# Kernel optimization log

Measured on AMD Instinct MI355X. Metric: run time of the kernel, lower is better.

The kernel has to match this reference:

```python
import jax, jax.numpy as jnp
import numpy as np

B, S, H, NH = 4, 2048, 768, 12
HD = H // NH

def _ln(x, g, b, eps=1e-5):
    m = jnp.mean(x, -1, keepdims=True)
    v = jnp.mean((x - m) ** 2, -1, keepdims=True)
    return (x - m) * jax.lax.rsqrt(v + eps) * g + b

def setup_inputs() -> dict:
    key = jax.random.key(0)
    ks = jax.random.split(key, 16)
    s = 0.02
    return {
        "x": jax.random.normal(ks[0], (B, S, H), jnp.float32),
        "prev_state": jax.random.normal(ks[1], (B, S, H), jnp.float32),
        "mask": jax.random.randint(ks[2], (B,), 0, 2).astype(bool),
        # depthwise conv1d (groups=H, k=3): torch weight [H, 1, 3] == OIH
        "conv_dw_w": jax.random.normal(ks[3], (H, 1, 3), jnp.float32) * s,
        "conv_dw_b": jnp.zeros((H,), jnp.float32),
        # pointwise conv1d (k=1) stored as [out, in]
        "conv_pw_w": jax.random.normal(ks[4], (H, H), jnp.float32) * s,
        "conv_pw_b": jnp.zeros((H,), jnp.float32),
        "cn_g": jnp.ones((H,), jnp.float32), "cn_b": jnp.zeros((H,), jnp.float32),
        "Wq": jax.random.normal(ks[5], (H, H), jnp.float32) * s, "bq": jnp.zeros((H,), jnp.float32),
        "Wk": jax.random.normal(ks[6], (H, H), jnp.float32) * s, "bk": jnp.zeros((H,), jnp.float32),
        "Wv": jax.random.normal(ks[7], (H, H), jnp.float32) * s, "bv": jnp.zeros((H,), jnp.float32),
        "Wo": jax.random.normal(ks[8], (H, H), jnp.float32) * s, "bo": jnp.zeros((H,), jnp.float32),
        "pn_g": jnp.ones((H,), jnp.float32), "pn_b": jnp.zeros((H,), jnp.float32),
        "Wpost": jax.random.normal(ks[9], (H, H), jnp.float32) * s, "bpost": jnp.zeros((H,), jnp.float32),
        "Wg": jax.random.normal(ks[10], (1, 2 * H), jnp.float32) * s, "bg": jnp.zeros((1,), jnp.float32),
    }

def reference(x, prev_state, mask, conv_dw_w, conv_dw_b, conv_pw_w, conv_pw_b,
              cn_g, cn_b, Wq, bq, Wk, bk, Wv, bv, Wo, bo,
              pn_g, pn_b, Wpost, bpost, Wg, bg):
    # ---- bridge: depthwise conv (k=3) -> pointwise conv (k=1) -> GELU -> LN ----
    mem_t = prev_state.transpose(0, 2, 1)  # [B, H, S]
    dw = jax.lax.conv_general_dilated(
        mem_t, conv_dw_w, window_strides=(1,), padding=[(1, 1)],
        feature_group_count=H, dimension_numbers=("NCH", "OIH", "NCH")) + conv_dw_b[None, :, None]
    pw = jnp.einsum("bhs,oh->bos", dw, conv_pw_w) + conv_pw_b[None, :, None]
    bridged = jax.nn.gelu(pw, approximate=False).transpose(0, 2, 1)  # [B, S, H]
    bridged = _ln(bridged, cn_g, cn_b)
    # ---- cross attention: q from x, k/v from bridged memory (nope, non-causal) ----
    q = (jnp.einsum("bsh,oh->bso", x, Wq) + bq).reshape(B, S, NH, HD)
    k = (jnp.einsum("bsh,oh->bso", bridged, Wk) + bk).reshape(B, S, NH, HD)
    v = (jnp.einsum("bsh,oh->bso", bridged, Wv) + bv).reshape(B, S, NH, HD)
    scores = jnp.einsum("bqnd,bknd->bnqk", q, k) / np.float32(np.sqrt(HD))
    attn = jax.nn.softmax(scores, axis=-1)
    ao = jnp.einsum("bnqk,bknd->bqnd", attn, v).reshape(B, S, H)
    ao = jnp.einsum("bsh,oh->bso", ao, Wo) + bo
    # ---- post-attn norm, linear, gate, scatter-add back under mask ----
    inj = _ln(ao, pn_g, pn_b)
    inj = jnp.einsum("bsh,oh->bso", inj, Wpost) + bpost
    gate = jax.nn.sigmoid(jnp.einsum("bsh,oh->bso", jnp.concatenate([x, bridged], -1), Wg) + bg)
    gated = gate * jnp.tanh(inj)
    mf = mask.astype(x.dtype)[:, None, None]  # batch-row select == masked scatter-add
    out = x + mf * gated
    # masked MSE aux loss (only over selected rows, as in the original)
    denom = jnp.maximum(mask.sum(), 1).astype(x.dtype) * np.float32(S * H)
    aux = jnp.sum(mf * (bridged - x) ** 2) / denom
    return out, aux
```

## Files before the change

kernel.cpp:

```cpp
#include <hip/hip_runtime.h>
#include <math.h>

#define B_ 4
#define S_ 2048
#define H_ 768
#define NH_ 12
#define HD_ 64
#define BSH (B_ * S_ * H_)
#define NROWS (B_ * S_)
#define WSZ (H_ * H_)

typedef __attribute__((ext_vector_type(8))) short bf16x8;
typedef __attribute__((ext_vector_type(4))) short s16x4;
typedef __attribute__((ext_vector_type(4))) float f32x4;
typedef __attribute__((ext_vector_type(2))) unsigned u32x2;

__device__ __forceinline__ short f2bf(float f) {
  union { float f; unsigned u; } x; x.f = f;
  unsigned r = x.u + 0x7FFF + ((x.u >> 16) & 1);
  return (short)(r >> 16);
}
__device__ __forceinline__ float bf2f(short s) {
  union { unsigned u; float f; } x;
  x.u = ((unsigned)(unsigned short)s) << 16;
  return x.f;
}
__device__ __forceinline__ unsigned bfpack(float lo, float hi) {
  union { float f; unsigned u; } a, b; a.f = lo; b.f = hi;
  return __builtin_amdgcn_perm(b.u, a.u, 0x07060302);
}

typedef __attribute__((address_space(1))) const unsigned int g_u32;
typedef __attribute__((address_space(3))) unsigned int l_u32;
__device__ __forceinline__ void gload16(const void* g, void* l) {
  __builtin_amdgcn_global_load_lds((g_u32*)g, (l_u32*)l, 16, 0, 0);
}

__global__ __launch_bounds__(256) void cvt_x_k(const float* __restrict__ src,
                                               short* __restrict__ dst) {
  int i = (blockIdx.x * 256 + threadIdx.x) * 4;
  float4 v = *(const float4*)(src + i);
  s16x4 o = {f2bf(v.x), f2bf(v.y), f2bf(v.z), f2bf(v.w)};
  *(s16x4*)(dst + i) = o;
}

__global__ __launch_bounds__(256) void cvt6_k(const float* w0, const float* w1,
                                              const float* w2, const float* w3,
                                              const float* w4, const float* w5,
                                              short* __restrict__ dst) {
  int i = (blockIdx.x * 256 + threadIdx.x) * 4;
  int m = i / WSZ;
  int off = i - m * WSZ;
  const float* s = m == 0 ? w0 : m == 1 ? w1 : m == 2 ? w2 : m == 3 ? w3 : m == 4 ? w4 : w5;
  float4 v = *(const float4*)(s + off);
  s16x4 o = {f2bf(v.x), f2bf(v.y), f2bf(v.z), f2bf(v.w)};
  *(s16x4*)(dst + i) = o;
}

__global__ __launch_bounds__(256) void dwconv_k(const float* __restrict__ prev,
                                                const float* __restrict__ w3,
                                                const float* __restrict__ bias,
                                                short* __restrict__ out) {
  int row = blockIdx.x;
  int s = row & (S_ - 1);
  size_t base = (size_t)row * H_;
  for (int h = threadIdx.x; h < H_; h += 256) {
    float acc = bias[h] + prev[base + h] * w3[h * 3 + 1];
    if (s > 0)      acc += prev[base - H_ + h] * w3[h * 3 + 0];
    if (s < S_ - 1) acc += prev[base + H_ + h] * w3[h * 3 + 2];
    out[base + h] = f2bf(acc);
  }
}

__global__ __launch_bounds__(256) void gemm_bf(const short* __restrict__ A,
                                               const short* __restrict__ W,
                                               const float* __restrict__ bias,
                                               short* __restrict__ C,
                                               int act, int tout) {
  __shared__ short As[4096];
  __shared__ short Ws[4096];
  int tid = threadIdx.x, lane = tid & 63, w = tid >> 6;
  int wr = w >> 1, wc = w & 1, lm = lane & 15, lq = lane >> 4;
  int m0 = blockIdx.y * 128, n0 = blockIdx.x * 128;
  int srow = w * 32 + (lane >> 2);
  int skc = (lane & 3) * 8;
  const short* gA = A + (size_t)(m0 + srow) * H_ + skc;
  const short* gW = W + (size_t)(n0 + srow) * H_ + skc;
  short* lA = As + w * 1024;
  short* lW = Ws + w * 1024;

  f32x4 acc[4][4];
#pragma unroll
  for (int i = 0; i < 4; ++i)
#pragma unroll
    for (int j = 0; j < 4; ++j) acc[i][j] = (f32x4){0.f, 0.f, 0.f, 0.f};

  for (int kt = 0; kt < H_; kt += 32) {
    __syncthreads();
    gload16(gA + kt, lA);
    gload16(gA + kt + 16 * H_, lA + 512);
    gload16(gW + kt, lW);
    gload16(gW + kt + 16 * H_, lW + 512);
    __syncthreads();
    bf16x8 af[4], wf[4];
#pragma unroll
    for (int i = 0; i < 4; ++i) af[i] = *(const bf16x8*)&As[(wr * 64 + i * 16 + lm) * 32 + lq * 8];
#pragma unroll
    for (int j = 0; j < 4; ++j) wf[j] = *(const bf16x8*)&Ws[(wc * 64 + j * 16 + lm) * 32 + lq * 8];
#pragma unroll
    for (int i = 0; i < 4; ++i)
#pragma unroll
      for (int j = 0; j < 4; ++j)
        acc[i][j] = __builtin_amdgcn_mfma_f32_16x16x32_bf16(af[i], wf[j], acc[i][j], 0, 0, 0);
  }

  if (!tout) {
#pragma unroll
    for (int j = 0; j < 4; ++j) {
      int col = n0 + wc * 64 + j * 16 + lm;
      float bn = bias[col];
#pragma unroll
      for (int i = 0; i < 4; ++i) {
        int mrow = m0 + wr * 64 + i * 16 + lq * 4;
#pragma unroll
        for (int r = 0; r < 4; ++r) {
          float cv = acc[i][j][r] + bn;
          if (act) cv = 0.5f * cv * (1.0f + erff(cv * 0.70710678118f));
          C[(size_t)(mrow + r) * H_ + col] = f2bf(cv);
        }
      }
    }
  } else {
    int b = m0 >> 11;
    int sb = (m0 & (S_ - 1)) + wr * 64;
#pragma unroll
    for (int j = 0; j < 4; ++j) {
      int col = n0 + wc * 64 + j * 16 + lm;
      float bn = bias[col];
      short* cp = C + ((size_t)(b * H_ + col)) * S_;
#pragma unroll
      for (int i = 0; i < 4; ++i) {
        int s = sb + i * 16 + lq * 4;
        s16x4 pk = {f2bf(acc[i][j][0] + bn), f2bf(acc[i][j][1] + bn),
                    f2bf(acc[i][j][2] + bn), f2bf(acc[i][j][3] + bn)};
        *(s16x4*)(cp + s) = pk;
      }
    }
  }
}

__global__ __launch_bounds__(256) void ln_bf(const short* __restrict__ X,
                                             short* __restrict__ Y,
                                             const float* __restrict__ g,
                                             const float* __restrict__ bb) {
  int row = blockIdx.x;
  size_t base = (size_t)row * H_;
  int h0 = threadIdx.x, h1 = h0 + 256, h2 = h0 + 512;
  float x0 = bf2f(X[base + h0]), x1 = bf2f(X[base + h1]), x2 = bf2f(X[base + h2]);
  float s = x0 + x1 + x2;
  float s2 = x0 * x0 + x1 * x1 + x2 * x2;
  for (int off = 32; off > 0; off >>= 1) {
    s += __shfl_down(s, off);
    s2 += __shfl_down(s2, off);
  }
  __shared__ float sa[4], sq[4], st[2];
  int wid = threadIdx.x >> 6, lane = threadIdx.x & 63;
  if (lane == 0) { sa[wid] = s; sq[wid] = s2; }
  __syncthreads();
  if (threadIdx.x == 0) {
    float ts = sa[0] + sa[1] + sa[2] + sa[3];
    float ts2 = sq[0] + sq[1] + sq[2] + sq[3];
    float mean = ts * (1.0f / H_);
    float var = ts2 * (1.0f / H_) - mean * mean;
    st[0] = mean;
    st[1] = rsqrtf(var + 1e-5f);
  }
  __syncthreads();
  float mean = st[0], rstd = st[1];
  Y[base + h0] = f2bf((x0 - mean) * rstd * g[h0] + bb[h0]);
  Y[base + h1] = f2bf((x1 - mean) * rstd * g[h1] + bb[h1]);
  Y[base + h2] = f2bf((x2 - mean) * rstd * g[h2] + bb[h2]);
}

__global__ __launch_bounds__(512) void attn3_k(const short* __restrict__ qb,
                                               const short* __restrict__ kb,
                                               const short* __restrict__ vtb,
                                               short* __restrict__ aob) {
  __shared__ short Ks[64 * 72];
  __shared__ short Vt[64 * 72];
  __shared__ short Ps[8 * 16 * 72];
  int tid = threadIdx.x, lane = tid & 63, w = tid >> 6;
  int lm = lane & 15, lq = lane >> 4;
  int b = blockIdx.z, n = blockIdx.y, q0 = blockIdx.x * 128;
  int hoff = n * HD_;

  const short* qrow = qb + ((size_t)(b * S_ + q0 + w * 16 + lm)) * H_ + hoff;
  bf16x8 qf0 = *(const bf16x8*)(qrow + lq * 8);
  bf16x8 qf1 = *(const bf16x8*)(qrow + 32 + lq * 8);

  float l_ = 0.f;
  f32x4 o[4];
#pragma unroll
  for (int i = 0; i < 4; ++i) o[i] = (f32x4){0.f, 0.f, 0.f, 0.f};

  int r0 = tid >> 3, c0 = (tid & 7) * 8;
  const short* kg = kb + ((size_t)(b * S_)) * H_ + hoff;
  const short* vg = vtb + ((size_t)(b * H_ + hoff)) * S_;
  const float C1 = 0.1803368802f;

  bf16x8 kv = *(const bf16x8*)(kg + (size_t)r0 * H_ + c0);
  bf16x8 vv = *(const bf16x8*)(vg + (size_t)r0 * S_ + c0);

  for (int kt = 0; kt < S_; kt += 64) {
    __syncthreads();
    *(bf16x8*)&Ks[r0 * 72 + c0] = kv;
    *(bf16x8*)&Vt[r0 * 72 + c0] = vv;
    __syncthreads();
    if (kt + 64 < S_) {
      kv = *(const bf16x8*)(kg + (size_t)(kt + 64 + r0) * H_ + c0);
      vv = *(const bf16x8*)(vg + (size_t)r0 * S_ + kt + 64 + c0);
    }

    f32x4 st[4];
#pragma unroll
    for (int ni = 0; ni < 4; ++ni) {
      bf16x8 ka0 = *(const bf16x8*)&Ks[(ni * 16 + lm) * 72 + lq * 8];
      bf16x8 ka1 = *(const bf16x8*)&Ks[(ni * 16 + lm) * 72 + 32 + lq * 8];
      f32x4 z = (f32x4){0.f, 0.f, 0.f, 0.f};
      z = __builtin_amdgcn_mfma_f32_16x16x32_bf16(ka0, qf0, z, 0, 0, 0);
      st[ni] = __builtin_amdgcn_mfma_f32_16x16x32_bf16(ka1, qf1, z, 0, 0, 0);
    }

    float rs = 0.f;
#pragma unroll
    for (int ni = 0; ni < 4; ++ni) {
      float p0 = exp2f(st[ni][0] * C1);
      float p1 = exp2f(st[ni][1] * C1);
      float p2 = exp2f(st[ni][2] * C1);
      float p3 = exp2f(st[ni][3] * C1);
      rs += (p0 + p1) + (p2 + p3);
      u32x2 pk = {bfpack(p0, p1), bfpack(p2, p3)};
      *(u32x2*)&Ps[(w * 16 + lm) * 72 + ni * 16 + lq * 4] = pk;
    }
    rs += __shfl_xor(rs, 16);
    rs += __shfl_xor(rs, 32);
    l_ += rs;

    bf16x8 pf0 = *(const bf16x8*)&Ps[(w * 16 + lm) * 72 + lq * 8];
    bf16x8 pf1 = *(const bf16x8*)&Ps[(w * 16 + lm) * 72 + 32 + lq * 8];
#pragma unroll
    for (int nd = 0; nd < 4; ++nd) {
      bf16x8 va0 = *(const bf16x8*)&Vt[(nd * 16 + lm) * 72 + lq * 8];
      bf16x8 va1 = *(const bf16x8*)&Vt[(nd * 16 + lm) * 72 + 32 + lq * 8];
      o[nd] = __builtin_amdgcn_mfma_f32_16x16x32_bf16(va0, pf0, o[nd], 0, 0, 0);
      o[nd] = __builtin_amdgcn_mfma_f32_16x16x32_bf16(va1, pf1, o[nd], 0, 0, 0);
    }
  }

  float inv = 1.0f / l_;
  short* orow = aob + ((size_t)(b * S_ + q0 + w * 16 + lm)) * H_ + hoff;
#pragma unroll
  for (int nd = 0; nd < 4; ++nd) {
    s16x4 pk = {f2bf(o[nd][0] * inv), f2bf(o[nd][1] * inv),
                f2bf(o[nd][2] * inv), f2bf(o[nd][3] * inv)};
    *(s16x4*)(orow + nd * 16 + lq * 4) = pk;
  }
}

__global__ __launch_bounds__(256) void gate_out_k(const float* __restrict__ x,
                                                  const short* __restrict__ br,
                                                  const short* __restrict__ inj,
                                                  const int* __restrict__ mask,
                                                  const float* __restrict__ Wg,
                                                  const float* __restrict__ bg,
                                                  float* __restrict__ out,
                                                  float* __restrict__ paux) {
  int row = blockIdx.x;
  int b = row >> 11;
  size_t base = (size_t)row * H_;
  float dot = 0.f, aux = 0.f;
  for (int h = threadIdx.x; h < H_; h += 256) {
    float xv = x[base + h], bv = bf2f(br[base + h]);
    dot += xv * Wg[h] + bv * Wg[H_ + h];
    float d = bv - xv;
    aux += d * d;
  }
  for (int off = 32; off > 0; off >>= 1) {
    dot += __shfl_down(dot, off);
    aux += __shfl_down(aux, off);
  }
  __shared__ float sd[4], sx[4], gsh[2];
  int wid = threadIdx.x >> 6, lane = threadIdx.x & 63;
  if (lane == 0) { sd[wid] = dot; sx[wid] = aux; }
  __syncthreads();
  if (threadIdx.x == 0) {
    float td = sd[0] + sd[1] + sd[2] + sd[3];
    float ta = sx[0] + sx[1] + sx[2] + sx[3];
    gsh[0] = 1.0f / (1.0f + expf(-(td + bg[0])));
    gsh[1] = ta;
  }
  __syncthreads();
  float mf = (mask[b] != 0) ? 1.0f : 0.0f;
  float gm = gsh[0] * mf;
  for (int h = threadIdx.x; h < H_; h += 256) {
    float v = bf2f(inj[base + h]);
    float e = __expf(2.0f * v);
    float th = (e - 1.0f) / (e + 1.0f);
    out[base + h] = x[base + h] + gm * th;
  }
  if (threadIdx.x == 0) paux[row] = mf * gsh[1];
}

__global__ __launch_bounds__(256) void aux_reduce_k(const float* __restrict__ paux,
                                                    const int* __restrict__ mask,
                                                    float* __restrict__ outp) {
  float s = 0.f;
  for (int i = threadIdx.x; i < NROWS; i += 256) s += paux[i];
  for (int off = 32; off > 0; off >>= 1) s += __shfl_down(s, off);
  __shared__ float sw[4];
  int wid = threadIdx.x >> 6, lane = threadIdx.x & 63;
  if (lane == 0) sw[wid] = s;
  __syncthreads();
  if (threadIdx.x == 0) {
    float t = sw[0] + sw[1] + sw[2] + sw[3];
    int nm = (mask[0] != 0) + (mask[1] != 0) + (mask[2] != 0) + (mask[3] != 0);
    if (nm < 1) nm = 1;
    outp[0] = t / ((float)nm * (float)(S_ * H_));
  }
}

extern "C" void kernel_launch(void* const* d_in, const int* in_sizes, int n_in,
                              void* d_out, int out_size, void* d_ws, size_t ws_size,
                              hipStream_t stream) {
  const float* x     = (const float*)d_in[0];
  const float* prev  = (const float*)d_in[1];
  const int*   mask  = (const int*)d_in[2];
  const float* dw_w  = (const float*)d_in[3];
  const float* dw_b  = (const float*)d_in[4];
  const float* pw_w  = (const float*)d_in[5];
  const float* pw_b  = (const float*)d_in[6];
  const float* cn_g  = (const float*)d_in[7];
  const float* cn_b  = (const float*)d_in[8];
  const float* Wq    = (const float*)d_in[9];
  const float* bq    = (const float*)d_in[10];
  const float* Wk    = (const float*)d_in[11];
  const float* bk    = (const float*)d_in[12];
  const float* Wv    = (const float*)d_in[13];
  const float* bv    = (const float*)d_in[14];
  const float* Wo    = (const float*)d_in[15];
  const float* bo    = (const float*)d_in[16];
  const float* pn_g  = (const float*)d_in[17];
  const float* pn_b  = (const float*)d_in[18];
  const float* Wpost = (const float*)d_in[19];
  const float* bpost = (const float*)d_in[20];
  const float* Wg    = (const float*)d_in[21];
  const float* bg    = (const float*)d_in[22];
  float* out = (float*)d_out;

  short* B0 = (short*)d_ws;
  short* B1 = B0 + BSH;
  short* B2 = B1 + BSH;
  short* B3 = B2 + BSH;
  short* B4 = B3 + BSH;
  short* B5 = B4 + BSH;
  short* WW = B5 + BSH;
  float* paux = (float*)(WW + 6 * WSZ);

  dim3 ggrid(H_ / 128, NROWS / 128);

  cvt6_k<<<6 * WSZ / 1024, 256, 0, stream>>>(pw_w, Wq, Wk, Wv, Wo, Wpost, WW);
  cvt_x_k<<<BSH / 1024, 256, 0, stream>>>(x, B0);
  dwconv_k<<<NROWS, 256, 0, stream>>>(prev, dw_w, dw_b, B1);
  gemm_bf<<<ggrid, 256, 0, stream>>>(B1, WW, pw_b, B2, 1, 0);
  ln_bf<<<NROWS, 256, 0, stream>>>(B2, B3, cn_g, cn_b);
  gemm_bf<<<ggrid, 256, 0, stream>>>(B0, WW + WSZ, bq, B1, 0, 0);
  gemm_bf<<<ggrid, 256, 0, stream>>>(B3, WW + 2 * WSZ, bk, B4, 0, 0);
  gemm_bf<<<ggrid, 256, 0, stream>>>(B3, WW + 3 * WSZ, bv, B5, 0, 1);
  attn3_k<<<dim3(S_ / 128, NH_, B_), 512, 0, stream>>>(B1, B4, B5, B2);
  gemm_bf<<<ggrid, 256, 0, stream>>>(B2, WW + 4 * WSZ, bo, B4, 0, 0);
  ln_bf<<<NROWS, 256, 0, stream>>>(B4, B4, pn_g, pn_b);
  gemm_bf<<<ggrid, 256, 0, stream>>>(B4, WW + 5 * WSZ, bpost, B5, 0, 0);
  gate_out_k<<<NROWS, 256, 0, stream>>>(x, B3, B5, mask, Wg, bg, out, paux);
  aux_reduce_k<<<1, 256, 0, stream>>>(paux, mask, out + BSH);
}
```

Measured before the change: 438.6 us.

## Batch QKV GEMMs in one launch, deepen K tile, vectorize elementwise kernels

The GEMM kernel now stages a 64-wide K slice per iteration instead of 32, which halves the number of barrier pairs. The Q, K and V projections are merged into a single launch using blockIdx.z to pick among three job descriptors. The depthwise conv and gate/output kernels now use 192 threads, each handling four contiguous elements with float4 and short4 loads instead of strided scalar loops. Together these aim to cut launch count, synchronisation overhead and memory instruction count, at the cost of twice the LDS per GEMM block, which may reduce occupancy.

```diff
diff --git a/kernel.cpp b/kernel.cpp
--- a/kernel.cpp
+++ b/kernel.cpp
@@ -57,76 +57,98 @@
   *(s16x4*)(dst + i) = o;
 }
 
-__global__ __launch_bounds__(256) void dwconv_k(const float* __restrict__ prev,
+__global__ __launch_bounds__(192) void dwconv_k(const float* __restrict__ prev,
                                                 const float* __restrict__ w3,
                                                 const float* __restrict__ bias,
                                                 short* __restrict__ out) {
   int row = blockIdx.x;
   int s = row & (S_ - 1);
-  size_t base = (size_t)row * H_;
-  for (int h = threadIdx.x; h < H_; h += 256) {
-    float acc = bias[h] + prev[base + h] * w3[h * 3 + 1];
-    if (s > 0)      acc += prev[base - H_ + h] * w3[h * 3 + 0];
-    if (s < S_ - 1) acc += prev[base + H_ + h] * w3[h * 3 + 2];
-    out[base + h] = f2bf(acc);
-  }
-}
-
-__global__ __launch_bounds__(256) void gemm_bf(const short* __restrict__ A,
-                                               const short* __restrict__ W,
-                                               const float* __restrict__ bias,
-                                               short* __restrict__ C,
-                                               int act, int tout) {
-  __shared__ short As[4096];
-  __shared__ short Ws[4096];
+  int h = threadIdx.x * 4;
+  size_t base = (size_t)row * H_ + h;
+  float4 c = *(const float4*)(prev + base);
+  float4 wa = *(const float4*)(w3 + h * 3);
+  float4 wb = *(const float4*)(w3 + h * 3 + 4);
+  float4 wc = *(const float4*)(w3 + h * 3 + 8);
+  float4 bi = *(const float4*)(bias + h);
+  float4 acc;
+  acc.x = bi.x + c.x * wa.y;
+  acc.y = bi.y + c.y * wb.x;
+  acc.z = bi.z + c.z * wb.w;
+  acc.w = bi.w + c.w * wc.z;
+  if (s > 0) {
+    float4 l = *(const float4*)(prev + base - H_);
+    acc.x += l.x * wa.x; acc.y += l.y * wa.w; acc.z += l.z * wb.z; acc.w += l.w * wc.y;
+  }
+  if (s < S_ - 1) {
+    float4 r = *(const float4*)(prev + base + H_);
+    acc.x += r.x * wa.z; acc.y += r.y * wb.y; acc.z += r.z * wc.x; acc.w += r.w * wc.w;
+  }
+  s16x4 o = {f2bf(acc.x), f2bf(acc.y), f2bf(acc.z), f2bf(acc.w)};
+  *(s16x4*)(out + base) = o;
+}
+
+struct GemmJob {
+  const short* A; const short* W; const float* bias; short* C; int act; int tout;
+};
+
+__global__ __launch_bounds__(256) void gemm_bf2(GemmJob j0, GemmJob j1, GemmJob j2) {
+  GemmJob j = blockIdx.z == 0 ? j0 : (blockIdx.z == 1 ? j1 : j2);
+  __shared__ short As[128 * 64];
+  __shared__ short Ws[128 * 64];
   int tid = threadIdx.x, lane = tid & 63, w = tid >> 6;
   int wr = w >> 1, wc = w & 1, lm = lane & 15, lq = lane >> 4;
   int m0 = blockIdx.y * 128, n0 = blockIdx.x * 128;
-  int srow = w * 32 + (lane >> 2);
-  int skc = (lane & 3) * 8;
-  const short* gA = A + (size_t)(m0 + srow) * H_ + skc;
-  const short* gW = W + (size_t)(n0 + srow) * H_ + skc;
-  short* lA = As + w * 1024;
-  short* lW = Ws + w * 1024;
+  int srow = lane >> 3;
+  int skc = (lane & 7) * 8;
+  const short* gA = j.A + (size_t)(m0 + w * 32 + srow) * H_ + skc;
+  const short* gW = j.W + (size_t)(n0 + w * 32 + srow) * H_ + skc;
+  short* lA = As + w * 2048;
+  short* lW = Ws + w * 2048;
 
   f32x4 acc[4][4];
 #pragma unroll
   for (int i = 0; i < 4; ++i)
 #pragma unroll
-    for (int j = 0; j < 4; ++j) acc[i][j] = (f32x4){0.f, 0.f, 0.f, 0.f};
-
-  for (int kt = 0; kt < H_; kt += 32) {
+    for (int jj = 0; jj < 4; ++jj) acc[i][jj] = (f32x4){0.f, 0.f, 0.f, 0.f};
+
+  for (int kt = 0; kt < H_; kt += 64) {
     __syncthreads();
-    gload16(gA + kt, lA);
-    gload16(gA + kt + 16 * H_, lA + 512);
-    gload16(gW + kt, lW);
-    gload16(gW + kt + 16 * H_, lW + 512);
+#pragma unroll
+    for (int c = 0; c < 4; ++c) {
+      gload16(gA + kt + (size_t)(c * 8) * H_, lA + c * 512);
+      gload16(gW + kt + (size_t)(c * 8) * H_, lW + c * 512);
+    }
     __syncthreads();
-    bf16x8 af[4], wf[4];
-#pragma unroll
-    for (int i = 0; i < 4; ++i) af[i] = *(const bf16x8*)&As[(wr * 64 + i * 16 + lm) * 32 + lq * 8];
-#pragma unroll
-    for (int j = 0; j < 4; ++j) wf[j] = *(const bf16x8*)&Ws[(wc * 64 + j * 16 + lm) * 32 + lq * 8];
-#pragma unroll
-    for (int i = 0; i < 4; ++i)
-#pragma unroll
-      for (int j = 0; j < 4; ++j)
-        acc[i][j] = __builtin_amdgcn_mfma_f32_16x16x32_bf16(af[i], wf[j], acc[i][j], 0, 0, 0);
-  }
-
-  if (!tout) {
-#pragma unroll
-    for (int j = 0; j < 4; ++j) {
-      int col = n0 + wc * 64 + j * 16 + lm;
-      float bn = bias[col];
+#pragma unroll
+    for (int kk = 0; kk < 2; ++kk) {
+      bf16x8 af[4], wf[4];
+#pragma unroll
+      for (int i = 0; i < 4; ++i)
+        af[i] = *(const bf16x8*)&As[(wr * 64 + i * 16 + lm) * 64 + kk * 32 + lq * 8];
+#pragma unroll
+      for (int jj = 0; jj < 4; ++jj)
+        wf[jj] = *(const bf16x8*)&Ws[(wc * 64 + jj * 16 + lm) * 64 + kk * 32 + lq * 8];
+#pragma unroll
+      for (int i = 0; i < 4; ++i)
+#pragma unroll
+        for (int jj = 0; jj < 4; ++jj)
+          acc[i][jj] = __builtin_amdgcn_mfma_f32_16x16x32_bf16(af[i], wf[jj], acc[i][jj], 0, 0, 0);
+    }
+  }
+
+  if (!j.tout) {
+#pragma unroll
+    for (int jj = 0; jj < 4; ++jj) {
+      int col = n0 + wc * 64 + jj * 16 + lm;
+      float bn = j.bias[col];
 #pragma unroll
       for (int i = 0; i < 4; ++i) {
         int mrow = m0 + wr * 64 + i * 16 + lq * 4;
 #pragma unroll
         for (int r = 0; r < 4; ++r) {
-          float cv = acc[i][j][r] + bn;
-          if (act) cv = 0.5f * cv * (1.0f + erff(cv * 0.70710678118f));
-          C[(size_t)(mrow + r) * H_ + col] = f2bf(cv);
+          float cv = acc[i][jj][r] + bn;
+          if (j.act) cv = 0.5f * cv * (1.0f + erff(cv * 0.70710678118f));
+          j.C[(size_t)(mrow + r) * H_ + col] = f2bf(cv);
         }
       }
     }
@@ -134,15 +156,15 @@
     int b = m0 >> 11;
     int sb = (m0 & (S_ - 1)) + wr * 64;
 #pragma unroll
-    for (int j = 0; j < 4; ++j) {
-      int col = n0 + wc * 64 + j * 16 + lm;
-      float bn = bias[col];
-      short* cp = C + ((size_t)(b * H_ + col)) * S_;
+    for (int jj = 0; jj < 4; ++jj) {
+      int col = n0 + wc * 64 + jj * 16 + lm;
+      float bn = j.bias[col];
+      short* cp = j.C + ((size_t)(b * H_ + col)) * S_;
 #pragma unroll
       for (int i = 0; i < 4; ++i) {
         int s = sb + i * 16 + lq * 4;
-        s16x4 pk = {f2bf(acc[i][j][0] + bn), f2bf(acc[i][j][1] + bn),
-                    f2bf(acc[i][j][2] + bn), f2bf(acc[i][j][3] + bn)};
+        s16x4 pk = {f2bf(acc[i][jj][0] + bn), f2bf(acc[i][jj][1] + bn),
+                    f2bf(acc[i][jj][2] + bn), f2bf(acc[i][jj][3] + bn)};
         *(s16x4*)(cp + s) = pk;
       }
     }
@@ -267,7 +289,7 @@
   }
 }
 
-__global__ __launch_bounds__(256) void gate_out_k(const float* __restrict__ x,
+__global__ __launch_bounds__(192) void gate_out_k(const float* __restrict__ x,
                                                   const short* __restrict__ br,
                                                   const short* __restrict__ inj,
                                                   const int* __restrict__ mask,
@@ -278,36 +300,42 @@
   int row = blockIdx.x;
   int b = row >> 11;
   size_t base = (size_t)row * H_;
-  float dot = 0.f, aux = 0.f;
-  for (int h = threadIdx.x; h < H_; h += 256) {
-    float xv = x[base + h], bv = bf2f(br[base + h]);
-    dot += xv * Wg[h] + bv * Wg[H_ + h];
-    float d = bv - xv;
-    aux += d * d;
-  }
+  int h = threadIdx.x * 4;
+  float4 xv = *(const float4*)(x + base + h);
+  s16x4 brv = *(const s16x4*)(br + base + h);
+  s16x4 inv = *(const s16x4*)(inj + base + h);
+  float4 wg0 = *(const float4*)(Wg + h);
+  float4 wg1 = *(const float4*)(Wg + H_ + h);
+  float b0 = bf2f(brv.x), b1 = bf2f(brv.y), b2 = bf2f(brv.z), b3 = bf2f(brv.w);
+  float dot = xv.x * wg0.x + xv.y * wg0.y + xv.z * wg0.z + xv.w * wg0.w
+            + b0 * wg1.x + b1 * wg1.y + b2 * wg1.z + b3 * wg1.w;
+  float d0 = b0 - xv.x, d1 = b1 - xv.y, d2 = b2 - xv.z, d3 = b3 - xv.w;
+  float aux = d0 * d0 + d1 * d1 + d2 * d2 + d3 * d3;
   for (int off = 32; off > 0; off >>= 1) {
     dot += __shfl_down(dot, off);
     aux += __shfl_down(aux, off);
   }
-  __shared__ float sd[4], sx[4], gsh[2];
+  __shared__ float sd[3], sx[3], gsh[2];
   int wid = threadIdx.x >> 6, lane = threadIdx.x & 63;
   if (lane == 0) { sd[wid] = dot; sx[wid] = aux; }
   __syncthreads();
   if (threadIdx.x == 0) {
-    float td = sd[0] + sd[1] + sd[2] + sd[3];
-    float ta = sx[0] + sx[1] + sx[2] + sx[3];
+    float td = sd[0] + sd[1] + sd[2];
+    float ta = sx[0] + sx[1] + sx[2];
     gsh[0] = 1.0f / (1.0f + expf(-(td + bg[0])));
     gsh[1] = ta;
   }
   __syncthreads();
   float mf = (mask[b] != 0) ? 1.0f : 0.0f;
   float gm = gsh[0] * mf;
-  for (int h = threadIdx.x; h < H_; h += 256) {
-    float v = bf2f(inj[base + h]);
-    float e = __expf(2.0f * v);
-    float th = (e - 1.0f) / (e + 1.0f);
-    out[base + h] = x[base + h] + gm * th;
-  }
+  float v0 = bf2f(inv.x), v1 = bf2f(inv.y), v2 = bf2f(inv.z), v3 = bf2f(inv.w);
+  float e0 = __expf(2.f * v0), e1 = __expf(2.f * v1), e2 = __expf(2.f * v2), e3 = __expf(2.f * v3);
+  float4 ov;
+  ov.x = xv.x + gm * ((e0 - 1.f) / (e0 + 1.f));
+  ov.y = xv.y + gm * ((e1 - 1.f) / (e1 + 1.f));
+  ov.z = xv.z + gm * ((e2 - 1.f) / (e2 + 1.f));
+  ov.w = xv.w + gm * ((e3 - 1.f) / (e3 + 1.f));
+  *(float4*)(out + base + h) = ov;
   if (threadIdx.x == 0) paux[row] = mf * gsh[1];
 }
 
@@ -366,20 +394,26 @@
   short* WW = B5 + BSH;
   float* paux = (float*)(WW + 6 * WSZ);
 
-  dim3 ggrid(H_ / 128, NROWS / 128);
+  dim3 g1(H_ / 128, NROWS / 128, 1);
+  dim3 g3(H_ / 128, NROWS / 128, 3);
+
+  GemmJob jpw   = {B1, WW,           pw_b,  B2, 1, 0};
+  GemmJob jq    = {B0, WW + WSZ,     bq,    B1, 0, 0};
+  GemmJob jk    = {B3, WW + 2 * WSZ, bk,    B4, 0, 0};
+  GemmJob jv    = {B3, WW + 3 * WSZ, bv,    B5, 0, 1};
+  GemmJob jo    = {B2, WW + 4 * WSZ, bo,    B4, 0, 0};
+  GemmJob jpost = {B4, WW + 5 * WSZ, bpost, B5, 0, 0};
 
   cvt6_k<<<6 * WSZ / 1024, 256, 0, stream>>>(pw_w, Wq, Wk, Wv, Wo, Wpost, WW);
   cvt_x_k<<<BSH / 1024, 256, 0, stream>>>(x, B0);
-  dwconv_k<<<NROWS, 256, 0, stream>>>(prev, dw_w, dw_b, B1);
-  gemm_bf<<<ggrid, 256, 0, stream>>>(B1, WW, pw_b, B2, 1, 0);
+  dwconv_k<<<NROWS, 192, 0, stream>>>(prev, dw_w, dw_b, B1);
+  gemm_bf2<<<g1, 256, 0, stream>>>(jpw, jpw, jpw);
   ln_bf<<<NROWS, 256, 0, stream>>>(B2, B3, cn_g, cn_b);
-  gemm_bf<<<ggrid, 256, 0, stream>>>(B0, WW + WSZ, bq, B1, 0, 0);
-  gemm_bf<<<ggrid, 256, 0, stream>>>(B3, WW + 2 * WSZ, bk, B4, 0, 0);
-  gemm_bf<<<ggrid, 256, 0, stream>>>(B3, WW + 3 * WSZ, bv, B5, 0, 1);
+  gemm_bf2<<<g3, 256, 0, stream>>>(jq, jk, jv);
   attn3_k<<<dim3(S_ / 128, NH_, B_), 512, 0, stream>>>(B1, B4, B5, B2);
-  gemm_bf<<<ggrid, 256, 0, stream>>>(B2, WW + 4 * WSZ, bo, B4, 0, 0);
+  gemm_bf2<<<g1, 256, 0, stream>>>(jo, jo, jo);
   ln_bf<<<NROWS, 256, 0, stream>>>(B4, B4, pn_g, pn_b);
-  gemm_bf<<<ggrid, 256, 0, stream>>>(B4, WW + 5 * WSZ, bpost, B5, 0, 0);
-  gate_out_k<<<NROWS, 256, 0, stream>>>(x, B3, B5, mask, Wg, bg, out, paux);
+  gemm_bf2<<<g1, 256, 0, stream>>>(jpost, jpost, jpost);
+  gate_out_k<<<NROWS, 192, 0, stream>>>(x, B3, B5, mask, Wg, bg, out, paux);
   aux_reduce_k<<<1, 256, 0, stream>>>(paux, mask, out + BSH);
 }
```

After: 419.2 us. 1.05x faster.
